# Kernel tuning notes

Measured on AMD Instinct MI355X. Metric: run time of the kernel, lower is better.

## Reference

```python
import jax, jax.numpy as jnp
import numpy as np

B, T, C, H = 2, 2048, 1024, 16
HD = C // H  # head dim = 64


def setup_inputs() -> dict:
    key = jax.random.key(0)
    ks = jax.random.split(key, 5)
    s = 0.02  # GPT-style init scale for weights
    return {
        "x": jax.random.normal(ks[0], (B, T, C), dtype=jnp.float32),
        "Wq": jax.random.normal(ks[1], (C, C), dtype=jnp.float32) * s,
        "bq": jnp.zeros((C,), dtype=jnp.float32),
        "Wk": jax.random.normal(ks[2], (C, C), dtype=jnp.float32) * s,
        "bk": jnp.zeros((C,), dtype=jnp.float32),
        "Wv": jax.random.normal(ks[3], (C, C), dtype=jnp.float32) * s,
        "bv": jnp.zeros((C,), dtype=jnp.float32),
        "Wp": jax.random.normal(ks[4], (C, C), dtype=jnp.float32) * s,
        "bp": jnp.zeros((C,), dtype=jnp.float32),
    }


def reference(x, Wq, bq, Wk, bk, Wv, bv, Wp, bp):
    b, t, c = x.shape
    # torch nn.Linear: y = x @ W.T + b  (W is [out, in])
    def heads(W, bias):
        y = jnp.einsum("btc,oc->bto", x, W) + bias
        return y.reshape(b, t, H, HD).transpose(0, 2, 1, 3)  # [B,H,T,hd]

    q = heads(Wq, bq)
    k = heads(Wk, bk)
    v = heads(Wv, bv)

    scale = 1.0 / np.sqrt(HD).astype(np.float32)
    att = jnp.einsum("bhqd,bhkd->bhqk", q, k) * scale  # [B,H,T,T]
    causal = jnp.tril(jnp.ones((t, t), dtype=bool))
    att = jnp.where(causal[None, None], att, -jnp.inf)
    att = jax.nn.softmax(att, axis=-1)
    # attn_pdrop = 0.0 -> dropout is identity
    y = jnp.einsum("bhqk,bhkd->bhqd", att, v)  # [B,H,T,hd]
    y = y.transpose(0, 2, 1, 3).reshape(b, t, c)
    y = jnp.einsum("btc,oc->bto", y, Wp) + bp  # resid_pdrop = 0.0
    return y
```

## Files before the change

kernel.cpp:

```cpp
#include <hip/hip_runtime.h>
#include <hip/hip_bf16.h>

using bf16 = __hip_bfloat16;
typedef __attribute__((ext_vector_type(8))) short short8;
typedef __attribute__((ext_vector_type(4))) float floatx4;

#define B_  2
#define T_  2048
#define C_  1024
#define H_  16
#define HD_ 64
#define BT_ (B_*T_)
#define NX_ ((size_t)BT_*C_)
#define NW_ ((size_t)C_*C_)
#define PSTR2 40
#define KSCQ 0.1803368801f

__device__ __forceinline__ void gl2lds16(const bf16* g, bf16* l) {
    __builtin_amdgcn_global_load_lds((const __attribute__((address_space(1))) unsigned int*)g,
                                     (__attribute__((address_space(3))) unsigned int*)l,
                                     16, 0, 0);
}

__global__ __launch_bounds__(256) void cvt_f32_bf16(
    const float* __restrict__ x,
    const float* __restrict__ Wq, const float* __restrict__ Wk,
    const float* __restrict__ Wv, const float* __restrict__ Wp,
    bf16* __restrict__ xb, bf16* __restrict__ wqb, bf16* __restrict__ wkb,
    bf16* __restrict__ wvb, bf16* __restrict__ wpb)
{
    size_t i4 = ((size_t)blockIdx.x * 256 + threadIdx.x) * 4;
    const float* src; bf16* dst; size_t off;
    if (i4 < NX_) { src = x; dst = xb; off = i4; }
    else {
        size_t j = i4 - NX_;
        int r = (int)(j >> 20);
        off = j & (NW_ - 1);
        src = (r==0) ? Wq : (r==1) ? Wk : (r==2) ? Wv : Wp;
        dst = (r==0) ? wqb : (r==1) ? wkb : (r==2) ? wvb : wpb;
    }
    float4 v = *(const float4*)(src + off);
    union { bf16 h[4]; uint2 u; } o;
    o.h[0] = __float2bfloat16(v.x); o.h[1] = __float2bfloat16(v.y);
    o.h[2] = __float2bfloat16(v.z); o.h[3] = __float2bfloat16(v.w);
    *(uint2*)(dst + off) = o.u;
}

__global__ __launch_bounds__(256) void qkv_gemm(
    const bf16* __restrict__ x,
    const bf16* __restrict__ Wq, const float* __restrict__ bq,
    const bf16* __restrict__ Wk, const float* __restrict__ bk,
    const bf16* __restrict__ Wv, const float* __restrict__ bv,
    bf16* __restrict__ qo, bf16* __restrict__ ko, bf16* __restrict__ vt)
{
    __shared__ __align__(16) bf16 As[128*32];
    __shared__ __align__(16) bf16 Bs[128*32];

    const int tid  = threadIdx.x;
    const int w    = tid >> 6, lane = tid & 63;
    const int g    = lane >> 4, c16 = lane & 15;
    const int wr   = w >> 1,    wc  = w & 1;
    const int mtile = blockIdx.x, ntile = blockIdx.y;
    const int wsel  = ntile >> 3;
    const bf16*  W    = (wsel==0) ? Wq : (wsel==1 ? Wk : Wv);
    const float* bias = (wsel==0) ? bq : (wsel==1 ? bk : bv);
    const float oscale = (wsel==0) ? KSCQ : 1.0f;
    const int nbase  = (ntile & 7) * 128;

    const bf16* ag = x + (size_t)(mtile*128)*C_;
    const bf16* bg = W + (size_t)nbase*C_;

    floatx4 acc[4][4] = {};

    for (int k0 = 0; k0 < C_; k0 += 32) {
        #pragma unroll
        for (int p = 0; p < 2; ++p) {
            int cb = p*256 + w*64;
            int c  = cb + lane;
            gl2lds16(ag + (size_t)(c>>2)*C_ + k0 + (c&3)*8, As + cb*8);
            gl2lds16(bg + (size_t)(c>>2)*C_ + k0 + (c&3)*8, Bs + cb*8);
        }
        __syncthreads();

        short8 af[4], bfr[4];
        #pragma unroll
        for (int i = 0; i < 4; ++i)
            af[i] = *(const short8*)(As + (wr*64 + i*16 + c16)*32 + g*8);
        #pragma unroll
        for (int j = 0; j < 4; ++j)
            bfr[j] = *(const short8*)(Bs + (wc*64 + j*16 + c16)*32 + g*8);
        #pragma unroll
        for (int i = 0; i < 4; ++i)
            #pragma unroll
            for (int j = 0; j < 4; ++j)
                acc[i][j] = __builtin_amdgcn_mfma_f32_16x16x32_bf16(af[i], bfr[j], acc[i][j], 0, 0, 0);
        __syncthreads();
    }

    #pragma unroll
    for (int i = 0; i < 4; ++i) {
        int m0 = mtile*128 + wr*64 + i*16 + g*4;
        #pragma unroll
        for (int j = 0; j < 4; ++j) {
            int n = nbase + wc*64 + j*16 + c16;
            float bvf = bias[n];
            if (wsel == 2) {
                int bb = m0 >> 11, t0 = m0 & (T_-1);
                int hh = n >> 6,  hd = n & 63;
                union { bf16 hv[4]; uint2 u; } tmp;
                #pragma unroll
                for (int r = 0; r < 4; ++r) tmp.hv[r] = __float2bfloat16(acc[i][j][r] + bvf);
                *(uint2*)(vt + ((size_t)((bb*H_ + hh)*64 + hd))*T_ + t0) = tmp.u;
            } else {
                bf16* dst = (wsel==0) ? qo : ko;
                #pragma unroll
                for (int r = 0; r < 4; ++r)
                    dst[(size_t)(m0+r)*C_ + n] = __float2bfloat16((acc[i][j][r] + bvf) * oscale);
            }
        }
    }
}

__global__ __launch_bounds__(512, 4) void attn(
    const bf16* __restrict__ q, const bf16* __restrict__ k,
    const bf16* __restrict__ vt, bf16* __restrict__ y)
{
    __shared__ __align__(16) bf16 Ks[16*512];
    __shared__ __align__(16) bf16 Vs[16*512];
    __shared__ __align__(16) bf16 Ps[8][16*PSTR2];

    const int tid = threadIdx.x, w = tid >> 6, lane = tid & 63;
    const int g = lane >> 4, c16 = lane & 15;
    const int wq = w & 3;
    const int kh = w >> 2;

    const int xcd = blockIdx.x & 7;
    const int j   = blockIdx.x >> 3;
    const int p   = j & 15;
    const int bh  = (j >> 4) * 8 + xcd;
    const int b = bh >> 4, h = bh & 15;

    const bf16* kbase = k  + ((size_t)(b*T_))*C_ + h*64;
    const bf16* vbase = vt + ((size_t)(b*H_ + h))*64*T_;

    const short ONEB = 0x3F80;
    const short8 ones = {ONEB,ONEB,ONEB,ONEB,ONEB,ONEB,ONEB,ONEB};

    for (int ph = 0; ph < 2; ++ph) {
        const int qt = ph ? 31 - p : p;
        const int qbase = qt*64 + wq*16;
        const int nit = (qt + 2) >> 1;
        const int qglob = qbase + c16;

        short8 aq[2];
        #pragma unroll
        for (int kg = 0; kg < 2; ++kg)
            aq[kg] = *(const short8*)(q + ((size_t)(b*T_ + qglob))*C_ + h*64 + kg*32 + g*8);

        floatx4 accO[4] = {};
        floatx4 lacc = {};

        for (int kt = 0; kt < nit; ++kt) {
            #pragma unroll
            for (int e = 0; e < 2; ++e) {
                int f = w*2 + e;
                gl2lds16(kbase + (size_t)(kt*128 + (f>>1)*16 + c16)*C_ + (f&1)*32 + g*8, Ks + f*512);
                gl2lds16(vbase + (size_t)((f&3)*16 + c16)*T_ + kt*128 + (f>>2)*32 + g*8, Vs + f*512);
            }
            __syncthreads();

            floatx4 s[4];
            __builtin_amdgcn_s_setprio(1);
            #pragma unroll
            for (int ct = 0; ct < 4; ++ct) {
                int ce = kh*4 + ct;
                short8 kb0 = *(const short8*)(Ks + (ce*2+0)*512 + lane*8);
                short8 kb1 = *(const short8*)(Ks + (ce*2+1)*512 + lane*8);
                floatx4 a = {0.f, 0.f, 0.f, 0.f};
                a = __builtin_amdgcn_mfma_f32_16x16x32_bf16(kb0, aq[0], a, 0, 0, 0);
                a = __builtin_amdgcn_mfma_f32_16x16x32_bf16(kb1, aq[1], a, 0, 0, 0);
                s[ct] = a;
            }
            __builtin_amdgcn_s_setprio(0);

            if (kt == nit-1) {
                #pragma unroll
                for (int ct = 0; ct < 4; ++ct)
                    #pragma unroll
                    for (int r = 0; r < 4; ++r) {
                        int key = kt*128 + kh*64 + ct*16 + g*4 + r;
                        if (key > qglob) s[ct][r] = -1e30f;
                    }
            }

            #pragma unroll
            for (int ks = 0; ks < 2; ++ks) {
                #pragma unroll
                for (int half = 0; half < 2; ++half) {
                    int ct = ks*2 + half;
                    float p0 = exp2f(s[ct][0]);
                    float p1 = exp2f(s[ct][1]);
                    float p2 = exp2f(s[ct][2]);
                    float p3 = exp2f(s[ct][3]);
                    union { __hip_bfloat162 h2[2]; uint2 u; } pk;
                    pk.h2[0] = __float22bfloat162_rn(float2{p0, p1});
                    pk.h2[1] = __float22bfloat162_rn(float2{p2, p3});
                    *(uint2*)(Ps[w] + c16*PSTR2 + half*16 + g*4) = pk.u;
                }
                short8 pa = *(const short8*)(Ps[w] + c16*PSTR2 + g*8);
                __builtin_amdgcn_s_setprio(1);
                lacc = __builtin_amdgcn_mfma_f32_16x16x32_bf16(pa, ones, lacc, 0, 0, 0);
                #pragma unroll
                for (int nt = 0; nt < 4; ++nt) {
                    short8 vb = *(const short8*)(Vs + ((kh*2 + ks)*4 + nt)*512 + lane*8);
                    accO[nt] = __builtin_amdgcn_mfma_f32_16x16x32_bf16(pa, vb, accO[nt], 0, 0, 0);
                }
                __builtin_amdgcn_s_setprio(0);
            }
            __syncthreads();
        }

        if (w >= 4) {
            float* dstf = ((w < 6) ? (float*)Ks : (float*)Vs) + (w & 1)*1280 + lane*20;
            #pragma unroll
            for (int nt = 0; nt < 4; ++nt) *(floatx4*)(dstf + nt*4) = accO[nt];
            *(floatx4*)(dstf + 16) = lacc;
        }
        __syncthreads();
        if (w < 4) {
            int pw = w + 4;
            const float* srcf = ((pw < 6) ? (const float*)Ks : (const float*)Vs) + (pw & 1)*1280 + lane*20;
            #pragma unroll
            for (int nt = 0; nt < 4; ++nt) {
                floatx4 o = *(const floatx4*)(srcf + nt*4);
                #pragma unroll
                for (int r = 0; r < 4; ++r) accO[nt][r] += o[r];
            }
            floatx4 lo = *(const floatx4*)(srcf + 16);
            #pragma unroll
            for (int r = 0; r < 4; ++r) lacc[r] += lo[r];

            float ir[4];
            #pragma unroll
            for (int r = 0; r < 4; ++r) ir[r] = __builtin_amdgcn_rcpf(lacc[r]);
            #pragma unroll
            for (int nt = 0; nt < 4; ++nt)
                #pragma unroll
                for (int r = 0; r < 4; ++r) {
                    int row = qbase + g*4 + r;
                    float o = accO[nt][r] * ir[r];
                    y[((size_t)(b*T_ + row))*C_ + h*64 + nt*16 + c16] = __float2bfloat16(o);
                }
        }
        __syncthreads();
    }
}

__global__ __launch_bounds__(256) void proj_gemm(
    const bf16* __restrict__ yin, const bf16* __restrict__ Wp, const float* __restrict__ bp,
    float* __restrict__ out)
{
    __shared__ __align__(16) bf16 As[64*32];
    __shared__ __align__(16) bf16 Bs[128*32];

    const int tid = threadIdx.x;
    const int w = tid >> 6, lane = tid & 63;
    const int g = lane >> 4, c16 = lane & 15;
    const int mtile = blockIdx.x, ntile = blockIdx.y;
    const int nbase = ntile * 128;

    const bf16* ag = yin + (size_t)(mtile*64)*C_;
    const bf16* bg = Wp  + (size_t)nbase*C_;

    floatx4 acc[4][2] = {};

    for (int k0 = 0; k0 < C_; k0 += 32) {
        gl2lds16(ag + (size_t)(w*16 + (lane>>2))*C_ + k0 + (lane&3)*8, As + w*512);
        #pragma unroll
        for (int p = 0; p < 2; ++p) {
            int cb = p*256 + w*64;
            int c  = cb + lane;
            gl2lds16(bg + (size_t)(c>>2)*C_ + k0 + (c&3)*8, Bs + cb*8);
        }
        __syncthreads();

        short8 af[4], bfr[2];
        #pragma unroll
        for (int i = 0; i < 4; ++i)
            af[i] = *(const short8*)(As + (i*16 + c16)*32 + g*8);
        #pragma unroll
        for (int j = 0; j < 2; ++j)
            bfr[j] = *(const short8*)(Bs + (w*32 + j*16 + c16)*32 + g*8);
        #pragma unroll
        for (int i = 0; i < 4; ++i)
            #pragma unroll
            for (int j = 0; j < 2; ++j)
                acc[i][j] = __builtin_amdgcn_mfma_f32_16x16x32_bf16(af[i], bfr[j], acc[i][j], 0, 0, 0);
        __syncthreads();
    }

    #pragma unroll
    for (int i = 0; i < 4; ++i) {
        int m0 = mtile*64 + i*16 + g*4;
        #pragma unroll
        for (int j = 0; j < 2; ++j) {
            int n = nbase + w*32 + j*16 + c16;
            float bvf = bp[n];
            #pragma unroll
            for (int r = 0; r < 4; ++r)
                out[(size_t)(m0+r)*C_ + n] = acc[i][j][r] + bvf;
        }
    }
}

extern "C" void kernel_launch(void* const* d_in, const int* in_sizes, int n_in,
                              void* d_out, int out_size, void* d_ws, size_t ws_size,
                              hipStream_t stream) {
    const float* x  = (const float*)d_in[0];
    const float* Wq = (const float*)d_in[1];
    const float* bq = (const float*)d_in[2];
    const float* Wk = (const float*)d_in[3];
    const float* bk = (const float*)d_in[4];
    const float* Wv = (const float*)d_in[5];
    const float* bv = (const float*)d_in[6];
    const float* Wp = (const float*)d_in[7];
    const float* bp = (const float*)d_in[8];

    bf16* xb  = (bf16*)d_ws;
    bf16* wqb = xb  + NX_;
    bf16* wkb = wqb + NW_;
    bf16* wvb = wkb + NW_;
    bf16* wpb = wvb + NW_;
    bf16* qw  = wpb + NW_;
    bf16* kw  = qw  + NX_;
    bf16* vt  = kw  + NX_;
    bf16* yw  = vt  + NX_;

    const int cvt_blocks = (int)((NX_ + 4*NW_) / (4*256));
    cvt_f32_bf16<<<cvt_blocks, 256, 0, stream>>>(x, Wq, Wk, Wv, Wp, xb, wqb, wkb, wvb, wpb);
    qkv_gemm<<<dim3(32, 24), 256, 0, stream>>>(xb, wqb, bq, wkb, bk, wvb, bv, qw, kw, vt);
    attn    <<<512, 512, 0, stream>>>(qw, kw, vt, yw);
    proj_gemm<<<dim3(64, 8), 256, 0, stream>>>(yw, wpb, bp, (float*)d_out);
}
```

Before: 183.3 us.

## Repartition attention waves to 2 query halves by 4 key quarters

Changes the attention kernel's wave split from 4 query groups by 2 key halves to 2 query groups of 32 rows by 4 key quarters. Each wave now handles two 16-row query tiles, so every K and V fragment read from LDS feeds two MFMAs instead of one. The cost is more partial results to combine: three waves write partials to LDS and the reduction runs once per query half, adding a barrier each time. It also swaps exp2f for the amdgcn exp2 builtin.

```diff
diff --git a/kernel.cpp b/kernel.cpp
--- a/kernel.cpp
+++ b/kernel.cpp
@@ -127,12 +127,12 @@
 {
     __shared__ __align__(16) bf16 Ks[16*512];
     __shared__ __align__(16) bf16 Vs[16*512];
-    __shared__ __align__(16) bf16 Ps[8][16*PSTR2];
+    __shared__ __align__(16) bf16 Ps[8][2][16*PSTR2];
 
     const int tid = threadIdx.x, w = tid >> 6, lane = tid & 63;
     const int g = lane >> 4, c16 = lane & 15;
-    const int wq = w & 3;
-    const int kh = w >> 2;
+    const int wq2 = w & 1;
+    const int kh4 = w >> 1;
 
     const int xcd = blockIdx.x & 7;
     const int j   = blockIdx.x >> 3;
@@ -148,17 +148,19 @@
 
     for (int ph = 0; ph < 2; ++ph) {
         const int qt = ph ? 31 - p : p;
-        const int qbase = qt*64 + wq*16;
         const int nit = (qt + 2) >> 1;
-        const int qglob = qbase + c16;
-
-        short8 aq[2];
-        #pragma unroll
-        for (int kg = 0; kg < 2; ++kg)
-            aq[kg] = *(const short8*)(q + ((size_t)(b*T_ + qglob))*C_ + h*64 + kg*32 + g*8);
-
-        floatx4 accO[4] = {};
-        floatx4 lacc = {};
+        const int qrow0 = qt*64 + wq2*32;
+        int qglob[2]; qglob[0] = qrow0 + c16; qglob[1] = qrow0 + 16 + c16;
+
+        short8 aq[2][2];
+        #pragma unroll
+        for (int qh = 0; qh < 2; ++qh)
+            #pragma unroll
+            for (int kg = 0; kg < 2; ++kg)
+                aq[qh][kg] = *(const short8*)(q + ((size_t)(b*T_ + qglob[qh]))*C_ + h*64 + kg*32 + g*8);
+
+        floatx4 accO[4][2] = {};
+        floatx4 lacc[2] = {};
 
         for (int kt = 0; kt < nit; ++kt) {
             #pragma unroll
@@ -169,90 +171,103 @@
             }
             __syncthreads();
 
-            floatx4 s[4];
+            floatx4 s[2][2];
             __builtin_amdgcn_s_setprio(1);
             #pragma unroll
-            for (int ct = 0; ct < 4; ++ct) {
-                int ce = kh*4 + ct;
+            for (int ct = 0; ct < 2; ++ct) {
+                int ce = kh4*2 + ct;
                 short8 kb0 = *(const short8*)(Ks + (ce*2+0)*512 + lane*8);
                 short8 kb1 = *(const short8*)(Ks + (ce*2+1)*512 + lane*8);
-                floatx4 a = {0.f, 0.f, 0.f, 0.f};
-                a = __builtin_amdgcn_mfma_f32_16x16x32_bf16(kb0, aq[0], a, 0, 0, 0);
-                a = __builtin_amdgcn_mfma_f32_16x16x32_bf16(kb1, aq[1], a, 0, 0, 0);
-                s[ct] = a;
+                #pragma unroll
+                for (int qh = 0; qh < 2; ++qh) {
+                    floatx4 a = {0.f, 0.f, 0.f, 0.f};
+                    a = __builtin_amdgcn_mfma_f32_16x16x32_bf16(kb0, aq[qh][0], a, 0, 0, 0);
+                    a = __builtin_amdgcn_mfma_f32_16x16x32_bf16(kb1, aq[qh][1], a, 0, 0, 0);
+                    s[qh][ct] = a;
+                }
             }
             __builtin_amdgcn_s_setprio(0);
 
             if (kt == nit-1) {
                 #pragma unroll
-                for (int ct = 0; ct < 4; ++ct)
+                for (int qh = 0; qh < 2; ++qh)
                     #pragma unroll
-                    for (int r = 0; r < 4; ++r) {
-                        int key = kt*128 + kh*64 + ct*16 + g*4 + r;
-                        if (key > qglob) s[ct][r] = -1e30f;
-                    }
-            }
-
-            #pragma unroll
-            for (int ks = 0; ks < 2; ++ks) {
-                #pragma unroll
-                for (int half = 0; half < 2; ++half) {
-                    int ct = ks*2 + half;
-                    float p0 = exp2f(s[ct][0]);
-                    float p1 = exp2f(s[ct][1]);
-                    float p2 = exp2f(s[ct][2]);
-                    float p3 = exp2f(s[ct][3]);
+                    for (int ct = 0; ct < 2; ++ct)
+                        #pragma unroll
+                        for (int r = 0; r < 4; ++r) {
+                            int key = kt*128 + kh4*32 + ct*16 + g*4 + r;
+                            if (key > qglob[qh]) s[qh][ct][r] = -1e30f;
+                        }
+            }
+
+            #pragma unroll
+            for (int qh = 0; qh < 2; ++qh) {
+                #pragma unroll
+                for (int ct = 0; ct < 2; ++ct) {
+                    float p0 = __builtin_amdgcn_exp2f(s[qh][ct][0]);
+                    float p1 = __builtin_amdgcn_exp2f(s[qh][ct][1]);
+                    float p2 = __builtin_amdgcn_exp2f(s[qh][ct][2]);
+                    float p3 = __builtin_amdgcn_exp2f(s[qh][ct][3]);
                     union { __hip_bfloat162 h2[2]; uint2 u; } pk;
                     pk.h2[0] = __float22bfloat162_rn(float2{p0, p1});
                     pk.h2[1] = __float22bfloat162_rn(float2{p2, p3});
-                    *(uint2*)(Ps[w] + c16*PSTR2 + half*16 + g*4) = pk.u;
+                    *(uint2*)(Ps[w][qh] + c16*PSTR2 + ct*16 + g*4) = pk.u;
                 }
-                short8 pa = *(const short8*)(Ps[w] + c16*PSTR2 + g*8);
-                __builtin_amdgcn_s_setprio(1);
-                lacc = __builtin_amdgcn_mfma_f32_16x16x32_bf16(pa, ones, lacc, 0, 0, 0);
-                #pragma unroll
-                for (int nt = 0; nt < 4; ++nt) {
-                    short8 vb = *(const short8*)(Vs + ((kh*2 + ks)*4 + nt)*512 + lane*8);
-                    accO[nt] = __builtin_amdgcn_mfma_f32_16x16x32_bf16(pa, vb, accO[nt], 0, 0, 0);
+            }
+            short8 pa0 = *(const short8*)(Ps[w][0] + c16*PSTR2 + g*8);
+            short8 pa1 = *(const short8*)(Ps[w][1] + c16*PSTR2 + g*8);
+            __builtin_amdgcn_s_setprio(1);
+            lacc[0] = __builtin_amdgcn_mfma_f32_16x16x32_bf16(pa0, ones, lacc[0], 0, 0, 0);
+            lacc[1] = __builtin_amdgcn_mfma_f32_16x16x32_bf16(pa1, ones, lacc[1], 0, 0, 0);
+            #pragma unroll
+            for (int nt = 0; nt < 4; ++nt) {
+                short8 vb = *(const short8*)(Vs + (kh4*4 + nt)*512 + lane*8);
+                accO[nt][0] = __builtin_amdgcn_mfma_f32_16x16x32_bf16(pa0, vb, accO[nt][0], 0, 0, 0);
+                accO[nt][1] = __builtin_amdgcn_mfma_f32_16x16x32_bf16(pa1, vb, accO[nt][1], 0, 0, 0);
+            }
+            __builtin_amdgcn_s_setprio(0);
+            __syncthreads();
+        }
+
+        #pragma unroll
+        for (int qh = 0; qh < 2; ++qh) {
+            if (w >= 2) {
+                int d = w - 2;
+                float* dstf = ((d < 3) ? (float*)Ks : (float*)Vs) + (d % 3)*1280 + lane*20;
+                #pragma unroll
+                for (int nt = 0; nt < 4; ++nt) *(floatx4*)(dstf + nt*4) = accO[nt][qh];
+                *(floatx4*)(dstf + 16) = lacc[qh];
+            }
+            __syncthreads();
+            if (w < 2) {
+                #pragma unroll
+                for (int kq = 1; kq < 4; ++kq) {
+                    int dw = kq*2 + wq2 - 2;
+                    const float* srcf = ((dw < 3) ? (const float*)Ks : (const float*)Vs) + (dw % 3)*1280 + lane*20;
+                    #pragma unroll
+                    for (int nt = 0; nt < 4; ++nt) {
+                        floatx4 o = *(const floatx4*)(srcf + nt*4);
+                        #pragma unroll
+                        for (int r = 0; r < 4; ++r) accO[nt][qh][r] += o[r];
+                    }
+                    floatx4 lo = *(const floatx4*)(srcf + 16);
+                    #pragma unroll
+                    for (int r = 0; r < 4; ++r) lacc[qh][r] += lo[r];
                 }
-                __builtin_amdgcn_s_setprio(0);
+                float ir[4];
+                #pragma unroll
+                for (int r = 0; r < 4; ++r) ir[r] = __builtin_amdgcn_rcpf(lacc[qh][r]);
+                #pragma unroll
+                for (int nt = 0; nt < 4; ++nt)
+                    #pragma unroll
+                    for (int r = 0; r < 4; ++r) {
+                        int row = qrow0 + qh*16 + g*4 + r;
+                        float o = accO[nt][qh][r] * ir[r];
+                        y[((size_t)(b*T_ + row))*C_ + h*64 + nt*16 + c16] = __float2bfloat16(o);
+                    }
             }
             __syncthreads();
         }
-
-        if (w >= 4) {
-            float* dstf = ((w < 6) ? (float*)Ks : (float*)Vs) + (w & 1)*1280 + lane*20;
-            #pragma unroll
-            for (int nt = 0; nt < 4; ++nt) *(floatx4*)(dstf + nt*4) = accO[nt];
-            *(floatx4*)(dstf + 16) = lacc;
-        }
-        __syncthreads();
-        if (w < 4) {
-            int pw = w + 4;
-            const float* srcf = ((pw < 6) ? (const float*)Ks : (const float*)Vs) + (pw & 1)*1280 + lane*20;
-            #pragma unroll
-            for (int nt = 0; nt < 4; ++nt) {
-                floatx4 o = *(const floatx4*)(srcf + nt*4);
-                #pragma unroll
-                for (int r = 0; r < 4; ++r) accO[nt][r] += o[r];
-            }
-            floatx4 lo = *(const floatx4*)(srcf + 16);
-            #pragma unroll
-            for (int r = 0; r < 4; ++r) lacc[r] += lo[r];
-
-            float ir[4];
-            #pragma unroll
-            for (int r = 0; r < 4; ++r) ir[r] = __builtin_amdgcn_rcpf(lacc[r]);
-            #pragma unroll
-            for (int nt = 0; nt < 4; ++nt)
-                #pragma unroll
-                for (int r = 0; r < 4; ++r) {
-                    int row = qbase + g*4 + r;
-                    float o = accO[nt][r] * ir[r];
-                    y[((size_t)(b*T_ + row))*C_ + h*64 + nt*16 + c16] = __float2bfloat16(o);
-                }
-        }
-        __syncthreads();
     }
 }
 
```

After: 186.1 us. No clear change (+1.5%).
